# Kernel tuning notes

Hardware: AMD Instinct MI355X
Metric: run time of the kernel (lower is better)

The kernel has to match this reference:

```python
import jax, jax.numpy as jnp
import numpy as np

B, S, D, H = 2, 2048, 1024, 16
HD = D // H

def setup_inputs() -> dict:
    key = jax.random.key(0)
    ks = jax.random.split(key, 6)
    s = 1.0 / np.sqrt(D)
    return {
        "inputs": jax.random.normal(ks[0], (B, S, D), dtype=jnp.float32),
        "Wq": jax.random.normal(ks[1], (D, D), dtype=jnp.float32) * s,
        "Wk": jax.random.normal(ks[2], (D, D), dtype=jnp.float32) * s,
        "Wv": jax.random.normal(ks[3], (D, D), dtype=jnp.float32) * s,
        "Wo": jax.random.normal(ks[4], (D, D), dtype=jnp.float32) * s,
        "bo": jax.random.normal(ks[5], (D,), dtype=jnp.float32) * 0.01,
    }

def reference(inputs, Wq, Wk, Wv, Wo, bo):
    b, n, _ = inputs.shape
    # Linear projections (torch Linear: x @ W.T), reshape to [b, H, n, hd]
    def proj(W):
        return (inputs @ W.T).reshape(b, n, H, HD).transpose(0, 2, 1, 3)
    q, k, v = proj(Wq), proj(Wk), proj(Wv)
    scores = jnp.einsum('bhqd,bhkd->bhqk', q, k)  # [b,H,n,n]
    causal = jnp.triu(jnp.ones((n, n), dtype=bool), k=1)
    scores = jnp.where(causal, -jnp.inf, scores)
    w = jax.nn.softmax(scores / np.sqrt(HD), axis=-1)
    ctx = jnp.einsum('bhqk,bhkd->bhqd', w, v)
    ctx = ctx.transpose(0, 2, 1, 3).reshape(b, n, D)
    return ctx @ Wo.T + bo
```

## Files before the change

kernel.cpp:

```cpp
#include <hip/hip_runtime.h>
#include <hip/hip_bf16.h>
#include <stdint.h>

#define B_   2
#define S_   2048
#define D_   1024
#define H_   16
#define LOG2E 1.4426950408889634f

using f32x4  = __attribute__((ext_vector_type(4))) float;
using short8 = __attribute__((ext_vector_type(8))) short;

__device__ __forceinline__ unsigned short f2bf(float x) {
    unsigned u = __builtin_bit_cast(unsigned, x);
    u += 0x7fffu + ((u >> 16) & 1u);
    return (unsigned short)(u >> 16);
}

__device__ __forceinline__ unsigned cvt_pk_bf16(float lo, float hi) {
    unsigned r;
    asm("v_cvt_pk_bf16_f32 %0, %1, %2" : "=v"(r) : "v"(lo), "v"(hi));
    return r;
}

__device__ __forceinline__ void gll16(const void* g, void* l) {
    __builtin_amdgcn_global_load_lds(
        (const __attribute__((address_space(1))) void*)(uintptr_t)g,
        (__attribute__((address_space(3))) void*)(uint32_t)(uintptr_t)l,
        16, 0, 0);
}

#define MFMA_BF16(a, b, c) __builtin_amdgcn_mfma_f32_16x16x32_bf16((a), (b), (c), 0, 0, 0)

__global__ __launch_bounds__(256)
void conv_all_kernel(const float* __restrict__ X,
                     const float* __restrict__ Wq, const float* __restrict__ Wk,
                     const float* __restrict__ Wv, const float* __restrict__ Wo,
                     short* __restrict__ Xb, short* __restrict__ Wqkv,
                     short* __restrict__ Wob) {
    const int bid = blockIdx.x;
    const float* src;
    short* dst;
    float sc = 1.0f;
    int i;
    if (bid < 2048) {
        src = X; dst = Xb; i = bid * 256 + threadIdx.x;
    } else {
        int wv = bid - 2048;
        int which = wv >> 9;
        src = (which == 0) ? Wq : (which == 1) ? Wk : (which == 2) ? Wv : Wo;
        dst = (which == 3) ? Wob : (Wqkv + (size_t)which * D_ * D_);
        if (which == 0) sc = 0.125f * LOG2E;
        i = (wv & 511) * 256 + threadIdx.x;
    }
    const float4* s4 = (const float4*)src;
    float4 a = s4[i * 2];
    float4 b = s4[i * 2 + 1];
    union { unsigned short u[8]; short8 v; } o;
    o.u[0] = f2bf(a.x * sc); o.u[1] = f2bf(a.y * sc); o.u[2] = f2bf(a.z * sc); o.u[3] = f2bf(a.w * sc);
    o.u[4] = f2bf(b.x * sc); o.u[5] = f2bf(b.y * sc); o.u[6] = f2bf(b.z * sc); o.u[7] = f2bf(b.w * sc);
    ((short8*)dst)[i] = o.v;
}

__global__ __launch_bounds__(512, 2)
void gemm_qkv256_kernel(const short* __restrict__ X, const short* __restrict__ Wqkv,
                        short* __restrict__ Qo, short* __restrict__ Ko,
                        short* __restrict__ VTo)
{
    __shared__ short sA[2][256 * 64];
    __shared__ short sB[2][256 * 64];
    const int cid = blockIdx.y * 12 + blockIdx.x;
    const int swz = (cid & 7) * 24 + (cid >> 3);
    const int n0 = (swz % 12) * 256;
    const int m0 = (swz / 12) * 256;
    const int tid = threadIdx.x, lane = tid & 63, w = tid >> 6;
    const int wm = w >> 2, wn = w & 3;
    const int l15 = lane & 15, lg = lane >> 4;

#define STAGE_T(buf, kt) do {                                                  \
        int k0_ = (kt) << 6;                                                   \
        _Pragma("unroll")                                                      \
        for (int it_ = 0; it_ < 4; ++it_) {                                    \
            int g_ = it_ * 512 + tid;                                          \
            int r_ = g_ >> 3, s_ = g_ & 7;                                     \
            int sb_ = s_ ^ (r_ & 7);                                           \
            int dst_ = (it_ * 512 + w * 64) * 16;                              \
            gll16(X    + (size_t)(m0 + r_) * D_ + k0_ + sb_ * 8,               \
                  (char*)sA[buf] + dst_);                                      \
            gll16(Wqkv + (size_t)(n0 + r_) * D_ + k0_ + sb_ * 8,               \
                  (char*)sB[buf] + dst_);                                      \
        }                                                                      \
    } while (0)

    const f32x4 z4 = {0.f, 0.f, 0.f, 0.f};
    f32x4 acc[8][4];
    #pragma unroll
    for (int i = 0; i < 8; ++i)
        #pragma unroll
        for (int j = 0; j < 4; ++j) acc[i][j] = z4;

    STAGE_T(0, 0);
    STAGE_T(1, 1);

    for (int t = 0; t < 16; ++t) {
        if (t < 15) { asm volatile("s_waitcnt vmcnt(8)" ::: "memory"); }
        else        { asm volatile("s_waitcnt vmcnt(0)" ::: "memory"); }
        __builtin_amdgcn_sched_barrier(0);
        __builtin_amdgcn_s_barrier();
        __builtin_amdgcn_sched_barrier(0);
        const short* a  = sA[t & 1];
        const short* bm = sB[t & 1];
        #pragma unroll
        for (int ks = 0; ks < 2; ++ks) {
            short8 af[8], bf[4];
            #pragma unroll
            for (int i = 0; i < 8; ++i) {
                int r = wm * 128 + i * 16 + l15;
                af[i] = *(const short8*)(a + r * 64 + ((((ks << 2) + lg) ^ (r & 7)) << 3));
            }
            #pragma unroll
            for (int j = 0; j < 4; ++j) {
                int r = wn * 64 + j * 16 + l15;
                bf[j] = *(const short8*)(bm + r * 64 + ((((ks << 2) + lg) ^ (r & 7)) << 3));
            }
            __builtin_amdgcn_s_setprio(1);
            #pragma unroll
            for (int i = 0; i < 8; ++i)
                #pragma unroll
                for (int j = 0; j < 4; ++j)
                    acc[i][j] = MFMA_BF16(af[i], bf[j], acc[i][j]);
            __builtin_amdgcn_s_setprio(0);
        }
        asm volatile("s_waitcnt lgkmcnt(0)" ::: "memory");
        __builtin_amdgcn_sched_barrier(0);
        __builtin_amdgcn_s_barrier();
        __builtin_amdgcn_sched_barrier(0);
        if (t + 2 < 16) STAGE_T(t & 1, t + 2);
    }
#undef STAGE_T

    const int z = n0 >> 10;
    if (z < 2) {
        short* Out = (z == 0) ? Qo : Ko;
        #pragma unroll
        for (int j = 0; j < 4; ++j) {
            int n = n0 + wn * 64 + j * 16 + l15;
            int h = (n >> 6) & 15, hd = n & 63;
            #pragma unroll
            for (int i = 0; i < 8; ++i)
                #pragma unroll
                for (int r = 0; r < 4; ++r) {
                    int m = m0 + wm * 128 + i * 16 + lg * 4 + r;
                    int b = m >> 11, s = m & (S_ - 1);
                    Out[(((size_t)b * H_ + h) * S_ + s) * 64 + hd] = (short)f2bf(acc[i][j][r]);
                }
        }
    } else {
        #pragma unroll
        for (int j = 0; j < 4; ++j) {
            int n = n0 + wn * 64 + j * 16 + l15;
            int h = (n >> 6) & 15, hd = n & 63;
            #pragma unroll
            for (int i = 0; i < 8; ++i) {
                int m = m0 + wm * 128 + i * 16 + lg * 4;
                int b = m >> 11, s0 = m & (S_ - 1);
                union { unsigned u32[2]; unsigned long long q64; } pk;
                pk.u32[0] = cvt_pk_bf16(acc[i][j][0], acc[i][j][1]);
                pk.u32[1] = cvt_pk_bf16(acc[i][j][2], acc[i][j][3]);
                *(unsigned long long*)(VTo + (((size_t)b * H_ + h) * 64 + hd) * S_ + s0) = pk.q64;
            }
        }
    }
}

__global__ __launch_bounds__(512, 2)
void gemm_out_kernel(const short* __restrict__ CTX, const short* __restrict__ Wob,
                     const float* __restrict__ bias, float* __restrict__ out)
{
    __shared__ short sA[2][128 * 64];
    __shared__ short sB[2][128 * 64];
    const int cid = blockIdx.y * 8 + blockIdx.x;
    const int swz = (cid & 7) * 32 + (cid >> 3);
    const int n0 = (swz & 7) * 128;
    const int m0 = (swz >> 3) * 128;
    const int tid = threadIdx.x, lane = tid & 63, w = tid >> 6;
    const int wm = w >> 2, wn = w & 3;
    const int l15 = lane & 15, lg = lane >> 4;

#define STAGE_O(buf, kt) do {                                                  \
        int k0_ = (kt) << 6;                                                   \
        _Pragma("unroll")                                                      \
        for (int it_ = 0; it_ < 2; ++it_) {                                    \
            int g_ = it_ * 512 + tid;                                          \
            int r_ = g_ >> 3, s_ = g_ & 7;                                     \
            int sb_ = s_ ^ (r_ & 7);                                           \
            int dst_ = (it_ * 512 + w * 64) * 16;                              \
            gll16(CTX + (size_t)(m0 + r_) * D_ + k0_ + sb_ * 8,                \
                  (char*)sA[buf] + dst_);                                      \
            gll16(Wob + (size_t)(n0 + r_) * D_ + k0_ + sb_ * 8,                \
                  (char*)sB[buf] + dst_);                                      \
        }                                                                      \
    } while (0)

    const f32x4 z4 = {0.f, 0.f, 0.f, 0.f};
    f32x4 acc[4][2];
    #pragma unroll
    for (int i = 0; i < 4; ++i)
        #pragma unroll
        for (int j = 0; j < 2; ++j) acc[i][j] = z4;

    STAGE_O(0, 0);
    STAGE_O(1, 1);

    for (int t = 0; t < 16; ++t) {
        if (t < 15) { asm volatile("s_waitcnt vmcnt(4)" ::: "memory"); }
        else        { asm volatile("s_waitcnt vmcnt(0)" ::: "memory"); }
        __builtin_amdgcn_sched_barrier(0);
        __builtin_amdgcn_s_barrier();
        __builtin_amdgcn_sched_barrier(0);
        const short* a  = sA[t & 1];
        const short* bm = sB[t & 1];
        #pragma unroll
        for (int ks = 0; ks < 2; ++ks) {
            short8 af[4], bf[2];
            #pragma unroll
            for (int i = 0; i < 4; ++i) {
                int r = wm * 64 + i * 16 + l15;
                af[i] = *(const short8*)(a + r * 64 + ((((ks << 2) + lg) ^ (r & 7)) << 3));
            }
            #pragma unroll
            for (int j = 0; j < 2; ++j) {
                int r = wn * 32 + j * 16 + l15;
                bf[j] = *(const short8*)(bm + r * 64 + ((((ks << 2) + lg) ^ (r & 7)) << 3));
            }
            __builtin_amdgcn_s_setprio(1);
            #pragma unroll
            for (int i = 0; i < 4; ++i)
                #pragma unroll
                for (int j = 0; j < 2; ++j)
                    acc[i][j] = MFMA_BF16(af[i], bf[j], acc[i][j]);
            __builtin_amdgcn_s_setprio(0);
        }
        asm volatile("s_waitcnt lgkmcnt(0)" ::: "memory");
        __builtin_amdgcn_sched_barrier(0);
        __builtin_amdgcn_s_barrier();
        __builtin_amdgcn_sched_barrier(0);
        if (t + 2 < 16) STAGE_O(t & 1, t + 2);
    }
#undef STAGE_O

    #pragma unroll
    for (int j = 0; j < 2; ++j) {
        int n = n0 + wn * 32 + j * 16 + l15;
        float bn = bias[n];
        #pragma unroll
        for (int i = 0; i < 4; ++i)
            #pragma unroll
            for (int r = 0; r < 4; ++r) {
                int m = m0 + wm * 64 + i * 16 + lg * 4 + r;
                out[(size_t)m * D_ + n] = acc[i][j][r] + bn;
            }
    }
}

__global__ __launch_bounds__(256, 4)
void attn_kernel(const short* __restrict__ Q, const short* __restrict__ K,
                 const short* __restrict__ VT, short* __restrict__ CTX)
{
    __shared__ short Kb[2][4096];
    __shared__ short Vb[2][4096];
    __shared__ char  Pl[4 * 2048];
    const int idx = blockIdx.x;
    const int p   = idx >> 7;
    const int q0  = (idx >> 5) & 3;
    const int bh  = idx & 31;
    const int b  = bh >> 4, h = bh & 15;
    const int tid = threadIdx.x, lane = tid & 63, w = tid >> 6;
    const int sx = w >> 1;
    const int l15 = lane & 15, lg = lane >> 4;
    const short* Qg = Q  + (size_t)bh * S_ * 64;
    const short* Kg = K  + (size_t)bh * S_ * 64;
    const short* Vg = VT + (size_t)bh * 64 * S_;
    char* Pw = Pl + w * 2048;

    const int qb = (sx ? (15 - p) : p) * 128 + q0 * 32 + (w & 1) * 16;
    const int nt = ((15 - p) * 128 + q0 * 32 + 31) / 64 + 1;

#define STAGE_KV(bufidx, ktile) do {                                         \
        int kt64_ = (ktile) << 6;                                            \
        _Pragma("unroll")                                                    \
        for (int it_ = 0; it_ < 2; ++it_) {                                  \
            int g_ = it_ * 256 + tid;                                        \
            int row_ = g_ >> 3, jb_ = g_ & 7;                                \
            int sj_ = jb_ ^ (row_ & 7);                                      \
            int base_ = (it_ * 256 + w * 64) * 16;                           \
            gll16(Kg + (size_t)(kt64_ + row_) * 64 + sj_ * 8,                \
                  (char*)Kb[bufidx] + base_);                                \
            gll16(Vg + (size_t)row_ * S_ + kt64_ + sj_ * 8,                  \
                  (char*)Vb[bufidx] + base_);                                \
        }                                                                    \
    } while (0)

    short8 qf[2];
    #pragma unroll
    for (int ks = 0; ks < 2; ++ks)
        qf[ks] = *(const short8*)(Qg + (size_t)(qb + l15) * 64 + ks * 32 + lg * 8);

    const short8 ones8 = { (short)0x3F80, (short)0x3F80, (short)0x3F80, (short)0x3F80,
                           (short)0x3F80, (short)0x3F80, (short)0x3F80, (short)0x3F80 };
    const f32x4 z4 = {0.f, 0.f, 0.f, 0.f};
    f32x4 o[4];
    f32x4 o5 = z4;
    #pragma unroll
    for (int nf = 0; nf < 4; ++nf) o[nf] = z4;

    STAGE_KV(0, 0);
    STAGE_KV(1, 1);

    for (int t = 0; t < nt; ++t) {
        if (t + 1 < nt) { asm volatile("s_waitcnt vmcnt(4)" ::: "memory"); }
        else            { asm volatile("s_waitcnt vmcnt(0)" ::: "memory"); }
        __builtin_amdgcn_sched_barrier(0);
        __builtin_amdgcn_s_barrier();
        __builtin_amdgcn_sched_barrier(0);
        const short* kb = Kb[t & 1];
        const short* vb = Vb[t & 1];
        const int kt = t << 6;

        if (kt <= qb + 15) {
            f32x4 sv[4] = {z4, z4, z4, z4};
            __builtin_amdgcn_s_setprio(1);
            #pragma unroll
            for (int ks = 0; ks < 2; ++ks)
                #pragma unroll
                for (int nf = 0; nf < 4; ++nf) {
                    int rr = nf * 16 + l15;
                    short8 kf = *(const short8*)((const char*)kb + rr * 128 +
                                                 (((ks << 2) + lg) ^ (rr & 7)) * 16);
                    sv[nf] = MFMA_BF16(kf, qf[ks], sv[nf]);
                }
            __builtin_amdgcn_s_setprio(0);
            if (kt + 63 > qb) {
                int q = qb + l15;
                #pragma unroll
                for (int nf = 0; nf < 4; ++nf)
                    #pragma unroll
                    for (int r = 0; r < 4; ++r)
                        if (kt + nf * 16 + lg * 4 + r > q) sv[nf][r] = -3e38f;
            }
            #pragma unroll
            for (int nf = 0; nf < 4; ++nf)
                #pragma unroll
                for (int r = 0; r < 4; ++r)
                    sv[nf][r] = exp2f(sv[nf][r]);
            #pragma unroll
            for (int nf = 0; nf < 4; ++nf) {
                union { unsigned u32[2]; unsigned long long q64; } pk;
                pk.u32[0] = cvt_pk_bf16(sv[nf][0], sv[nf][1]);
                pk.u32[1] = cvt_pk_bf16(sv[nf][2], sv[nf][3]);
                int kby = (nf * 16 + lg * 4) * 2;
                int off = l15 * 128 + (((kby >> 4) ^ (l15 & 7)) << 4) + (kby & 15);
                *(unsigned long long*)(Pw + off) = pk.q64;
            }
            #pragma unroll
            for (int ks = 0; ks < 2; ++ks) {
                int off = l15 * 128 + ((((ks << 2) + lg) ^ (l15 & 7)) << 4);
                short8 af = *(const short8*)(Pw + off);
                __builtin_amdgcn_s_setprio(1);
                #pragma unroll
                for (int nf = 0; nf < 4; ++nf) {
                    int rr = nf * 16 + l15;
                    short8 vf = *(const short8*)((const char*)vb + rr * 128 +
                                                 (((ks << 2) + lg) ^ (rr & 7)) * 16);
                    o[nf] = MFMA_BF16(af, vf, o[nf]);
                }
                o5 = MFMA_BF16(af, ones8, o5);
                __builtin_amdgcn_s_setprio(0);
            }
        }
        asm volatile("s_waitcnt lgkmcnt(0)" ::: "memory");
        __builtin_amdgcn_sched_barrier(0);
        __builtin_amdgcn_s_barrier();
        __builtin_amdgcn_sched_barrier(0);
        if (t + 2 < nt) STAGE_KV(t & 1, t + 2);
    }
#undef STAGE_KV

    #pragma unroll
    for (int r = 0; r < 4; ++r) {
        float inv = 1.0f / o5[r];
        int s = qb + lg * 4 + r;
        size_t base = ((size_t)b * S_ + s) * D_ + h * 64;
        #pragma unroll
        for (int nf = 0; nf < 4; ++nf)
            CTX[base + nf * 16 + l15] = (short)f2bf(o[nf][r] * inv);
    }
}

extern "C" void kernel_launch(void* const* d_in, const int* in_sizes, int n_in,
                              void* d_out, int out_size, void* d_ws, size_t ws_size,
                              hipStream_t stream) {
    const float* X  = (const float*)d_in[0];
    const float* Wq = (const float*)d_in[1];
    const float* Wk = (const float*)d_in[2];
    const float* Wv = (const float*)d_in[3];
    const float* Wo = (const float*)d_in[4];
    const float* bo = (const float*)d_in[5];
    float* out = (float*)d_out;

    char* ws = (char*)d_ws;
    const size_t MB = 1024 * 1024;
    short* Xb   = (short*)(ws);
    short* CTXw = (short*)(ws);
    short* Wqkv = (short*)(ws +  8 * MB);
    short* Wob  = (short*)(ws + 14 * MB);
    short* Qw   = (short*)(ws + 16 * MB);
    short* Kw   = (short*)(ws + 24 * MB);
    short* VTw  = (short*)(ws + 32 * MB);

    conv_all_kernel<<<4096, 256, 0, stream>>>(X, Wq, Wk, Wv, Wo, Xb, Wqkv, Wob);

    gemm_qkv256_kernel<<<dim3(12, 16), 512, 0, stream>>>(Xb, Wqkv, Qw, Kw, VTw);

    attn_kernel<<<1024, 256, 0, stream>>>(Qw, Kw, VTw, CTXw);

    gemm_out_kernel<<<dim3(8, 32), 512, 0, stream>>>(CTXw, Wob, bo, out);
}
```

Before: 105.1 us.

## Shrink QKV GEMM tiles to 128x128, raise occupancy, use raw exp/rcp

The QKV projection GEMM drops from 256x256 to 128x128 output tiles, launched as 768 blocks instead of 192, with launch bounds raised to 4 blocks per CU. This fills the CUs better and allows more concurrent waves, at the cost of less operand reuse per tile. The out-projection GEMM gets the same launch-bound change. In attention, exp2f and the reciprocal are replaced with raw v_exp_f32 and v_rcp_f32 to drop range-handling and precise-division overhead, at a small accuracy cost.

```diff
diff --git a/kernel.cpp b/kernel.cpp
--- a/kernel.cpp
+++ b/kernel.cpp
@@ -20,6 +20,18 @@
 __device__ __forceinline__ unsigned cvt_pk_bf16(float lo, float hi) {
     unsigned r;
     asm("v_cvt_pk_bf16_f32 %0, %1, %2" : "=v"(r) : "v"(lo), "v"(hi));
+    return r;
+}
+
+__device__ __forceinline__ float fast_exp2(float x) {
+    float r;
+    asm("v_exp_f32 %0, %1" : "=v"(r) : "v"(x));
+    return r;
+}
+
+__device__ __forceinline__ float fast_rcp(float x) {
+    float r;
+    asm("v_rcp_f32 %0, %1" : "=v"(r) : "v"(x));
     return r;
 }
 
@@ -62,25 +74,25 @@
     ((short8*)dst)[i] = o.v;
 }
 
-__global__ __launch_bounds__(512, 2)
-void gemm_qkv256_kernel(const short* __restrict__ X, const short* __restrict__ Wqkv,
+__global__ __launch_bounds__(512, 4)
+void gemm_qkv128_kernel(const short* __restrict__ X, const short* __restrict__ Wqkv,
                         short* __restrict__ Qo, short* __restrict__ Ko,
                         short* __restrict__ VTo)
 {
-    __shared__ short sA[2][256 * 64];
-    __shared__ short sB[2][256 * 64];
-    const int cid = blockIdx.y * 12 + blockIdx.x;
-    const int swz = (cid & 7) * 24 + (cid >> 3);
-    const int n0 = (swz % 12) * 256;
-    const int m0 = (swz / 12) * 256;
+    __shared__ short sA[2][128 * 64];
+    __shared__ short sB[2][128 * 64];
+    const int cid = blockIdx.x;
+    const int swz = (cid & 7) * 96 + (cid >> 3);
+    const int n0 = (swz % 24) * 128;
+    const int m0 = (swz / 24) * 128;
     const int tid = threadIdx.x, lane = tid & 63, w = tid >> 6;
     const int wm = w >> 2, wn = w & 3;
     const int l15 = lane & 15, lg = lane >> 4;
 
-#define STAGE_T(buf, kt) do {                                                  \
+#define STAGE_Q(buf, kt) do {                                                  \
         int k0_ = (kt) << 6;                                                   \
         _Pragma("unroll")                                                      \
-        for (int it_ = 0; it_ < 4; ++it_) {                                    \
+        for (int it_ = 0; it_ < 2; ++it_) {                                    \
             int g_ = it_ * 512 + tid;                                          \
             int r_ = g_ >> 3, s_ = g_ & 7;                                     \
             int sb_ = s_ ^ (r_ & 7);                                           \
@@ -93,17 +105,17 @@
     } while (0)
 
     const f32x4 z4 = {0.f, 0.f, 0.f, 0.f};
-    f32x4 acc[8][4];
-    #pragma unroll
-    for (int i = 0; i < 8; ++i)
-        #pragma unroll
-        for (int j = 0; j < 4; ++j) acc[i][j] = z4;
-
-    STAGE_T(0, 0);
-    STAGE_T(1, 1);
+    f32x4 acc[4][2];
+    #pragma unroll
+    for (int i = 0; i < 4; ++i)
+        #pragma unroll
+        for (int j = 0; j < 2; ++j) acc[i][j] = z4;
+
+    STAGE_Q(0, 0);
+    STAGE_Q(1, 1);
 
     for (int t = 0; t < 16; ++t) {
-        if (t < 15) { asm volatile("s_waitcnt vmcnt(8)" ::: "memory"); }
+        if (t < 15) { asm volatile("s_waitcnt vmcnt(4)" ::: "memory"); }
         else        { asm volatile("s_waitcnt vmcnt(0)" ::: "memory"); }
         __builtin_amdgcn_sched_barrier(0);
         __builtin_amdgcn_s_barrier();
@@ -112,22 +124,22 @@
         const short* bm = sB[t & 1];
         #pragma unroll
         for (int ks = 0; ks < 2; ++ks) {
-            short8 af[8], bf[4];
-            #pragma unroll
-            for (int i = 0; i < 8; ++i) {
-                int r = wm * 128 + i * 16 + l15;
+            short8 af[4], bf[2];
+            #pragma unroll
+            for (int i = 0; i < 4; ++i) {
+                int r = wm * 64 + i * 16 + l15;
                 af[i] = *(const short8*)(a + r * 64 + ((((ks << 2) + lg) ^ (r & 7)) << 3));
             }
             #pragma unroll
-            for (int j = 0; j < 4; ++j) {
-                int r = wn * 64 + j * 16 + l15;
+            for (int j = 0; j < 2; ++j) {
+                int r = wn * 32 + j * 16 + l15;
                 bf[j] = *(const short8*)(bm + r * 64 + ((((ks << 2) + lg) ^ (r & 7)) << 3));
             }
             __builtin_amdgcn_s_setprio(1);
             #pragma unroll
-            for (int i = 0; i < 8; ++i)
-                #pragma unroll
-                for (int j = 0; j < 4; ++j)
+            for (int i = 0; i < 4; ++i)
+                #pragma unroll
+                for (int j = 0; j < 2; ++j)
                     acc[i][j] = MFMA_BF16(af[i], bf[j], acc[i][j]);
             __builtin_amdgcn_s_setprio(0);
         }
@@ -135,34 +147,34 @@
         __builtin_amdgcn_sched_barrier(0);
         __builtin_amdgcn_s_barrier();
         __builtin_amdgcn_sched_barrier(0);
-        if (t + 2 < 16) STAGE_T(t & 1, t + 2);
-    }
-#undef STAGE_T
+        if (t + 2 < 16) STAGE_Q(t & 1, t + 2);
+    }
+#undef STAGE_Q
 
     const int z = n0 >> 10;
     if (z < 2) {
         short* Out = (z == 0) ? Qo : Ko;
         #pragma unroll
-        for (int j = 0; j < 4; ++j) {
-            int n = n0 + wn * 64 + j * 16 + l15;
+        for (int j = 0; j < 2; ++j) {
+            int n = n0 + wn * 32 + j * 16 + l15;
             int h = (n >> 6) & 15, hd = n & 63;
             #pragma unroll
-            for (int i = 0; i < 8; ++i)
+            for (int i = 0; i < 4; ++i)
                 #pragma unroll
                 for (int r = 0; r < 4; ++r) {
-                    int m = m0 + wm * 128 + i * 16 + lg * 4 + r;
+                    int m = m0 + wm * 64 + i * 16 + lg * 4 + r;
                     int b = m >> 11, s = m & (S_ - 1);
                     Out[(((size_t)b * H_ + h) * S_ + s) * 64 + hd] = (short)f2bf(acc[i][j][r]);
                 }
         }
     } else {
         #pragma unroll
-        for (int j = 0; j < 4; ++j) {
-            int n = n0 + wn * 64 + j * 16 + l15;
+        for (int j = 0; j < 2; ++j) {
+            int n = n0 + wn * 32 + j * 16 + l15;
             int h = (n >> 6) & 15, hd = n & 63;
             #pragma unroll
-            for (int i = 0; i < 8; ++i) {
-                int m = m0 + wm * 128 + i * 16 + lg * 4;
+            for (int i = 0; i < 4; ++i) {
+                int m = m0 + wm * 64 + i * 16 + lg * 4;
                 int b = m >> 11, s0 = m & (S_ - 1);
                 union { unsigned u32[2]; unsigned long long q64; } pk;
                 pk.u32[0] = cvt_pk_bf16(acc[i][j][0], acc[i][j][1]);
@@ -173,7 +185,7 @@
     }
 }
 
-__global__ __launch_bounds__(512, 2)
+__global__ __launch_bounds__(512, 4)
 void gemm_out_kernel(const short* __restrict__ CTX, const short* __restrict__ Wob,
                      const float* __restrict__ bias, float* __restrict__ out)
 {
@@ -352,7 +364,7 @@
             for (int nf = 0; nf < 4; ++nf)
                 #pragma unroll
                 for (int r = 0; r < 4; ++r)
-                    sv[nf][r] = exp2f(sv[nf][r]);
+                    sv[nf][r] = fast_exp2(sv[nf][r]);
             #pragma unroll
             for (int nf = 0; nf < 4; ++nf) {
                 union { unsigned u32[2]; unsigned long long q64; } pk;
@@ -388,7 +400,7 @@
 
     #pragma unroll
     for (int r = 0; r < 4; ++r) {
-        float inv = 1.0f / o5[r];
+        float inv = fast_rcp(o5[r]);
         int s = qb + lg * 4 + r;
         size_t base = ((size_t)b * S_ + s) * D_ + h * 64;
         #pragma unroll
@@ -420,7 +432,7 @@
 
     conv_all_kernel<<<4096, 256, 0, stream>>>(X, Wq, Wk, Wv, Wo, Xb, Wqkv, Wob);
 
-    gemm_qkv256_kernel<<<dim3(12, 16), 512, 0, stream>>>(Xb, Wqkv, Qw, Kw, VTw);
+    gemm_qkv128_kernel<<<768, 512, 0, stream>>>(Xb, Wqkv, Qw, Kw, VTw);
 
     attn_kernel<<<1024, 256, 0, stream>>>(Qw, Kw, VTw, CTXw);
 
```

After: 89.35 us. -15.0%, faster.

## Deepen QKV GEMM pipeline, use raw exp/rcp in attention, raise out-GEMM occupancy

Applied to the files above, without the earlier changes.

The QKV projection GEMM moves from a 2-stage, K=64 LDS pipeline to a 4-stage, K=32 pipeline. Loads for A and B are split and interleaved with two halves of the MFMA work, so global-to-LDS traffic overlaps compute with only one barrier per step. The attention kernel replaces exp2f and the division by hardware v_exp_f32 and v_rcp_f32, which drop denormal and range handling. The output GEMM's launch bounds now request 4 waves-per-EU occupancy, which may force register spilling.

```diff
diff --git a/kernel.cpp b/kernel.cpp
--- a/kernel.cpp
+++ b/kernel.cpp
@@ -20,6 +20,18 @@
 __device__ __forceinline__ unsigned cvt_pk_bf16(float lo, float hi) {
     unsigned r;
     asm("v_cvt_pk_bf16_f32 %0, %1, %2" : "=v"(r) : "v"(lo), "v"(hi));
+    return r;
+}
+
+__device__ __forceinline__ float fast_exp2(float x) {
+    float r;
+    asm("v_exp_f32 %0, %1" : "=v"(r) : "v"(x));
+    return r;
+}
+
+__device__ __forceinline__ float fast_rcp(float x) {
+    float r;
+    asm("v_rcp_f32 %0, %1" : "=v"(r) : "v"(x));
     return r;
 }
 
@@ -67,9 +79,9 @@
                         short* __restrict__ Qo, short* __restrict__ Ko,
                         short* __restrict__ VTo)
 {
-    __shared__ short sA[2][256 * 64];
-    __shared__ short sB[2][256 * 64];
-    const int cid = blockIdx.y * 12 + blockIdx.x;
+    __shared__ short sA[4][256 * 32];
+    __shared__ short sB[4][256 * 32];
+    const int cid = blockIdx.x;
     const int swz = (cid & 7) * 24 + (cid >> 3);
     const int n0 = (swz % 12) * 256;
     const int m0 = (swz / 12) * 256;
@@ -77,20 +89,28 @@
     const int wm = w >> 2, wn = w & 3;
     const int l15 = lane & 15, lg = lane >> 4;
 
-#define STAGE_T(buf, kt) do {                                                  \
-        int k0_ = (kt) << 6;                                                   \
+#define STG_A(buf, kt) do {                                                    \
+        int k0_ = (kt) << 5;                                                   \
         _Pragma("unroll")                                                      \
-        for (int it_ = 0; it_ < 4; ++it_) {                                    \
+        for (int it_ = 0; it_ < 2; ++it_) {                                    \
             int g_ = it_ * 512 + tid;                                          \
-            int r_ = g_ >> 3, s_ = g_ & 7;                                     \
-            int sb_ = s_ ^ (r_ & 7);                                           \
-            int dst_ = (it_ * 512 + w * 64) * 16;                              \
-            gll16(X    + (size_t)(m0 + r_) * D_ + k0_ + sb_ * 8,               \
-                  (char*)sA[buf] + dst_);                                      \
-            gll16(Wqkv + (size_t)(n0 + r_) * D_ + k0_ + sb_ * 8,               \
-                  (char*)sB[buf] + dst_);                                      \
+            int r_ = g_ >> 2, s_ = g_ & 3;                                     \
+            int sb_ = s_ ^ ((r_ >> 1) & 3);                                    \
+            gll16(X + (size_t)(m0 + r_) * D_ + k0_ + sb_ * 8,                  \
+                  (char*)sA[buf] + (it_ * 512 + w * 64) * 16);                 \
         }                                                                      \
     } while (0)
+#define STG_B(buf, kt) do {                                                    \
+        int k0_ = (kt) << 5;                                                   \
+        _Pragma("unroll")                                                      \
+        for (int it_ = 0; it_ < 2; ++it_) {                                    \
+            int g_ = it_ * 512 + tid;                                          \
+            int r_ = g_ >> 2, s_ = g_ & 3;                                     \
+            int sb_ = s_ ^ ((r_ >> 1) & 3);                                    \
+            gll16(Wqkv + (size_t)(n0 + r_) * D_ + k0_ + sb_ * 8,               \
+                  (char*)sB[buf] + (it_ * 512 + w * 64) * 16);                 \
+        }                                                                      \
+    } while (0)
 
     const f32x4 z4 = {0.f, 0.f, 0.f, 0.f};
     f32x4 acc[8][4];
@@ -99,45 +119,61 @@
         #pragma unroll
         for (int j = 0; j < 4; ++j) acc[i][j] = z4;
 
-    STAGE_T(0, 0);
-    STAGE_T(1, 1);
-
-    for (int t = 0; t < 16; ++t) {
-        if (t < 15) { asm volatile("s_waitcnt vmcnt(8)" ::: "memory"); }
-        else        { asm volatile("s_waitcnt vmcnt(0)" ::: "memory"); }
+    STG_A(0, 0); STG_B(0, 0);
+    STG_A(1, 1); STG_B(1, 1);
+    STG_A(2, 2); STG_B(2, 2);
+    asm volatile("s_waitcnt vmcnt(8)" ::: "memory");
+    __builtin_amdgcn_sched_barrier(0);
+    __builtin_amdgcn_s_barrier();
+    __builtin_amdgcn_sched_barrier(0);
+
+    for (int t = 0; t < 32; ++t) {
+        const short* a  = sA[t & 3];
+        const short* bm = sB[t & 3];
+        short8 af[8], bf[4];
+        #pragma unroll
+        for (int i = 0; i < 4; ++i) {
+            int r = wm * 128 + i * 16 + l15;
+            af[i] = *(const short8*)(a + r * 32 + ((lg ^ ((r >> 1) & 3)) << 3));
+        }
+        #pragma unroll
+        for (int j = 0; j < 4; ++j) {
+            int r = wn * 64 + j * 16 + l15;
+            bf[j] = *(const short8*)(bm + r * 32 + ((lg ^ ((r >> 1) & 3)) << 3));
+        }
+        if (t + 3 < 32) STG_A((t + 3) & 3, t + 3);
+        asm volatile("s_waitcnt lgkmcnt(0)" ::: "memory");
+        __builtin_amdgcn_sched_barrier(0);
+        __builtin_amdgcn_s_setprio(1);
+        #pragma unroll
+        for (int i = 0; i < 4; ++i)
+            #pragma unroll
+            for (int j = 0; j < 4; ++j)
+                acc[i][j] = MFMA_BF16(af[i], bf[j], acc[i][j]);
+        __builtin_amdgcn_s_setprio(0);
+        #pragma unroll
+        for (int i = 4; i < 8; ++i) {
+            int r = wm * 128 + i * 16 + l15;
+            af[i] = *(const short8*)(a + r * 32 + ((lg ^ ((r >> 1) & 3)) << 3));
+        }
+        if (t + 3 < 32) STG_B((t + 3) & 3, t + 3);
+        if (t <= 28)      { asm volatile("s_waitcnt vmcnt(8)" ::: "memory"); }
+        else if (t == 29) { asm volatile("s_waitcnt vmcnt(4)" ::: "memory"); }
+        else              { asm volatile("s_waitcnt vmcnt(0)" ::: "memory"); }
+        asm volatile("s_waitcnt lgkmcnt(0)" ::: "memory");
         __builtin_amdgcn_sched_barrier(0);
         __builtin_amdgcn_s_barrier();
         __builtin_amdgcn_sched_barrier(0);
-        const short* a  = sA[t & 1];
-        const short* bm = sB[t & 1];
-        #pragma unroll
-        for (int ks = 0; ks < 2; ++ks) {
-            short8 af[8], bf[4];
-            #pragma unroll
-            for (int i = 0; i < 8; ++i) {
-                int r = wm * 128 + i * 16 + l15;
-                af[i] = *(const short8*)(a + r * 64 + ((((ks << 2) + lg) ^ (r & 7)) << 3));
-            }
-            #pragma unroll
-            for (int j = 0; j < 4; ++j) {
-                int r = wn * 64 + j * 16 + l15;
-                bf[j] = *(const short8*)(bm + r * 64 + ((((ks << 2) + lg) ^ (r & 7)) << 3));
-            }
-            __builtin_amdgcn_s_setprio(1);
-            #pragma unroll
-            for (int i = 0; i < 8; ++i)
-                #pragma unroll
-                for (int j = 0; j < 4; ++j)
-                    acc[i][j] = MFMA_BF16(af[i], bf[j], acc[i][j]);
-            __builtin_amdgcn_s_setprio(0);
-        }
-        asm volatile("s_waitcnt lgkmcnt(0)" ::: "memory");
-        __builtin_amdgcn_sched_barrier(0);
-        __builtin_amdgcn_s_barrier();
-        __builtin_amdgcn_sched_barrier(0);
-        if (t + 2 < 16) STAGE_T(t & 1, t + 2);
-    }
-#undef STAGE_T
+        __builtin_amdgcn_s_setprio(1);
+        #pragma unroll
+        for (int i = 4; i < 8; ++i)
+            #pragma unroll
+            for (int j = 0; j < 4; ++j)
+                acc[i][j] = MFMA_BF16(af[i], bf[j], acc[i][j]);
+        __builtin_amdgcn_s_setprio(0);
+    }
+#undef STG_A
+#undef STG_B
 
     const int z = n0 >> 10;
     if (z < 2) {
@@ -173,7 +209,7 @@
     }
 }
 
-__global__ __launch_bounds__(512, 2)
+__global__ __launch_bounds__(512, 4)
 void gemm_out_kernel(const short* __restrict__ CTX, const short* __restrict__ Wob,
                      const float* __restrict__ bias, float* __restrict__ out)
 {
@@ -352,7 +388,7 @@
             for (int nf = 0; nf < 4; ++nf)
                 #pragma unroll
                 for (int r = 0; r < 4; ++r)
-                    sv[nf][r] = exp2f(sv[nf][r]);
+                    sv[nf][r] = fast_exp2(sv[nf][r]);
             #pragma unroll
             for (int nf = 0; nf < 4; ++nf) {
                 union { unsigned u32[2]; unsigned long long q64; } pk;
@@ -388,7 +424,7 @@
 
     #pragma unroll
     for (int r = 0; r < 4; ++r) {
-        float inv = 1.0f / o5[r];
+        float inv = fast_rcp(o5[r]);
         int s = qb + lg * 4 + r;
         size_t base = ((size_t)b * S_ + s) * D_ + h * 64;
         #pragma unroll
@@ -420,7 +456,7 @@
 
     conv_all_kernel<<<4096, 256, 0, stream>>>(X, Wq, Wk, Wv, Wo, Xb, Wqkv, Wob);
 
-    gemm_qkv256_kernel<<<dim3(12, 16), 512, 0, stream>>>(Xb, Wqkv, Qw, Kw, VTw);
+    gemm_qkv256_kernel<<<192, 512, 0, stream>>>(Xb, Wqkv, Qw, Kw, VTw);
 
     attn_kernel<<<1024, 256, 0, stream>>>(Qw, Kw, VTw, CTXw);
 
```

Result: faster. 92.18 us (-12.3%).
